# Optimization experiments

Measured on AMD Instinct MI355X. Metric: run time of the kernel, lower is better.

## Reference

```python
import jax, jax.numpy as jnp
import numpy as np

NUM_EMBEDDINGS = 256
EMBEDDING_DIM = 8


def setup_inputs() -> dict:
    key = jax.random.key(0)
    ks = jax.random.split(key, 8)
    B, D_in, H, D_out = 1024, 512, 2048, 512
    s = lambda fan: 1.0 / np.sqrt(fan)
    return {
        "x": jax.random.normal(ks[0], (B, D_in), dtype=jnp.float32),
        "emb_W": jax.random.normal(ks[1], (NUM_EMBEDDINGS, EMBEDDING_DIM), dtype=jnp.float32),
        "W_in": jax.random.normal(ks[2], (H, D_in), dtype=jnp.float32) * s(D_in),
        "b_in": jax.random.normal(ks[3], (H,), dtype=jnp.float32) * s(D_in),
        "W_h": jax.random.normal(ks[4], (H, H), dtype=jnp.float32) * s(H),
        "b_h": jax.random.normal(ks[5], (H,), dtype=jnp.float32) * s(H),
        "W_out": jax.random.normal(ks[6], (D_out, H), dtype=jnp.float32) * s(H),
        "b_out": jax.random.normal(ks[7], (D_out,), dtype=jnp.float32) * s(H),
    }


def reference(x, emb_W, W_in, b_in, W_h, b_h, W_out, b_out):
    B, D_in = x.shape
    flat = x.reshape(-1)  # [B*D_in], row-major flatten == torch .flatten()
    # power-feature expansion: powers 1..embedding_dim stacked on axis 1
    exps = jnp.arange(1, EMBEDDING_DIM + 1, dtype=x.dtype)
    x_res = flat[:, None] ** exps[None, :]  # [B*D_in, E]
    # get_ind: NOTE source uses sum(flat_x) (not sum of squares) -- faithful
    sm = jnp.sum(x_res, axis=1, keepdims=True)              # [N,1]
    emb = jnp.sum(emb_W * emb_W, axis=1)[None, :]           # [1,K]
    dist = sm + emb - 2.0 * (x_res @ emb_W.T)               # [N,K]
    ind = jnp.argmin(dist, axis=1)                          # [N] int
    # q = ind.view_as(x.T).T : reshape to [D_in, B] then transpose
    q = ind.reshape(D_in, B).T.astype(x.dtype)              # [B, D_in]
    # straight-through: forward value q, gradient flows to x
    q = x + jax.lax.stop_gradient(q - x)
    relu = jax.nn.relu
    h = relu(q @ W_in.T + b_in)      # d_in
    for _ in range(4):               # shared d_h applied 4 times
        h = relu(h @ W_h.T + b_h)
    f = relu(h @ W_out.T + b_out)    # d_out
    q_latent_loss = jnp.float32(0.0)  # eval mode
    return (f, q_latent_loss)
```

## Files before the change

### kernel.cpp

```cpp
#include <hip/hip_runtime.h>
#include <hip/hip_bf16.h>
#include <math.h>


#define B_ROWS 1024
#define D_IN   512
#define HDIM   2048
#define NTOT   (B_ROWS * D_IN)
#define NCODE  256
#define EDIM   8

typedef __attribute__((ext_vector_type(8))) short bf16x8;
typedef __attribute__((ext_vector_type(4))) float f32x4;

__device__ inline void gload_lds16(const void* g, void* l) {
    __builtin_amdgcn_global_load_lds(
        (const __attribute__((address_space(1))) void*)g,
        (__attribute__((address_space(3))) void*)l, 16, 0, 0);
}

__device__ inline ushort bf16_hi_bits(float v, float* hi_f) {
    __hip_bfloat16 h = __float2bfloat16(v);
    *hi_f = __bfloat162float(h);
    ushort u; __builtin_memcpy(&u, &h, 2); return u;
}
__device__ inline ushort bf16_bits(float v) {
    __hip_bfloat16 h = __float2bfloat16(v);
    ushort u; __builtin_memcpy(&u, &h, 2); return u;
}

__global__ __launch_bounds__(256) void quantize_kernel(
    const float* __restrict__ x, const float* __restrict__ embW,
    ushort* __restrict__ qhi, float* __restrict__ loss_out)
{
    __shared__ float sW[NCODE][EDIM];
    __shared__ float sE[NCODE];

    const int tid = threadIdx.x;
    for (int i = tid; i < NCODE * EDIM; i += 256)
        ((float*)sW)[i] = embW[i];
    __syncthreads();
    {
        const float* w = sW[tid];
        float s0 = __fmul_rn(w[0], w[0]), s1 = __fmul_rn(w[1], w[1]);
        float s2 = __fmul_rn(w[2], w[2]), s3 = __fmul_rn(w[3], w[3]);
        float s4 = __fmul_rn(w[4], w[4]), s5 = __fmul_rn(w[5], w[5]);
        float s6 = __fmul_rn(w[6], w[6]), s7 = __fmul_rn(w[7], w[7]);
        float a = __fadd_rn(__fadd_rn(s0, s1), __fadd_rn(s2, s3));
        float b = __fadd_rn(__fadd_rn(s4, s5), __fadd_rn(s6, s7));
        sE[tid] = __fadd_rn(a, b);
    }
    __syncthreads();

    const int n = blockIdx.x * 256 + tid;
    const float v = x[n];

    float p[EDIM];
    #pragma unroll
    for (int e = 0; e < EDIM; ++e)
        p[e] = powf(v, (float)(e + 1));

    float sm;
    {
        float a = __fadd_rn(__fadd_rn(p[0], p[1]), __fadd_rn(p[2], p[3]));
        float b = __fadd_rn(__fadd_rn(p[4], p[5]), __fadd_rn(p[6], p[7]));
        sm = __fadd_rn(a, b);
    }

    float best = INFINITY;
    int bi = 0;
    for (int k = 0; k < NCODE; ++k) {
        const float4 w0 = *reinterpret_cast<const float4*>(&sW[k][0]);
        const float4 w1 = *reinterpret_cast<const float4*>(&sW[k][4]);
        float dot = 0.f;
        dot = fmaf(p[0], w0.x, dot); dot = fmaf(p[1], w0.y, dot);
        dot = fmaf(p[2], w0.z, dot); dot = fmaf(p[3], w0.w, dot);
        dot = fmaf(p[4], w1.x, dot); dot = fmaf(p[5], w1.y, dot);
        dot = fmaf(p[6], w1.z, dot); dot = fmaf(p[7], w1.w, dot);
        float d = __fsub_rn(__fadd_rn(sm, sE[k]), __fmul_rn(2.0f, dot));
        if (d < best) { best = d; bi = k; }
    }

    const int bo = n & (B_ROWS - 1);
    const int dd = n >> 10;
    qhi[bo * D_IN + dd] = bf16_bits((float)bi);

    if (blockIdx.x == 0 && tid == 0) loss_out[0] = 0.0f;
}

__global__ __launch_bounds__(256) void split_all(
    const float* __restrict__ Wi, const float* __restrict__ Wh,
    const float* __restrict__ Wo,
    ushort* __restrict__ wihi, ushort* __restrict__ wilo,
    ushort* __restrict__ whhi, ushort* __restrict__ whlo,
    ushort* __restrict__ wohi, ushort* __restrict__ wolo)
{
    const int i = blockIdx.x * 256 + threadIdx.x;
    const int R0 = HDIM * D_IN / 4;
    const int R1 = R0 + HDIM * HDIM / 4;
    const float* src; ushort* hi; ushort* lo; int j;
    if (i < R0)      { src = Wi; hi = wihi; lo = wilo; j = i; }
    else if (i < R1) { src = Wh; hi = whhi; lo = whlo; j = i - R0; }
    else             { src = Wo; hi = wohi; lo = wolo; j = i - R1; }
    float4 v = reinterpret_cast<const float4*>(src)[j];
    float f[4] = {v.x, v.y, v.z, v.w};
    ushort hh[4], ll[4];
    #pragma unroll
    for (int c = 0; c < 4; ++c) {
        float hf;
        hh[c] = bf16_hi_bits(f[c], &hf);
        ll[c] = bf16_bits(f[c] - hf);
    }
    ushort4 h = {hh[0], hh[1], hh[2], hh[3]};
    ushort4 l = {ll[0], ll[1], ll[2], ll[3]};
    reinterpret_cast<ushort4*>(hi)[j] = h;
    reinterpret_cast<ushort4*>(lo)[j] = l;
}

template<bool ALO, bool PARTIAL>
__global__ __launch_bounds__(256) void gemm_split(
    const ushort* __restrict__ Ahi, const ushort* __restrict__ Alo,
    const ushort* __restrict__ Whi, const ushort* __restrict__ Wlo,
    const float* __restrict__ bias,
    ushort* __restrict__ Ohi, ushort* __restrict__ Olo,
    float* __restrict__ OF, int N, int K, int klen)
{
    constexpr int BUF = 49152;
    constexpr int OFF_AH = 0, OFF_AL = 8192, OFF_BH = 16384;
    __shared__ char lds[2 * BUF];

    const int tid = threadIdx.x, lane = tid & 63, wid = tid >> 6;

    const int gy = gridDim.y;
    const int nwg = gridDim.x * gy;
    int lin = blockIdx.x * gy + blockIdx.y;
    int q   = nwg >> 3;
    int sw  = (lin & 7) * q + (lin >> 3);
    int bx  = sw / gy, by2 = sw % gy;
    const int bm   = (by2 & 15) << 6;
    const int kz   = by2 >> 4;
    const int kbeg = kz * klen;
    const int bn   = bx << 7;

    const int wm = (wid >> 1) << 5;
    const int wn = (wid & 1) << 6;

    constexpr int NSEGW = ALO ? 12 : 10;
    const ushort* gp[NSEGW];
    uint ldsoff[NSEGW];
    #pragma unroll
    for (int i = 0; i < NSEGW; ++i) {
        int s = wid + i * 4;
        const ushort* pl; int row0, base, sip;
        if (ALO) {
            if (s < 8)       { pl = Ahi; row0 = bm; base = OFF_AH;         sip = s; }
            else if (s < 16) { pl = Alo; row0 = bm; base = OFF_AL;         sip = s - 8; }
            else if (s < 32) { pl = Whi; row0 = bn; base = OFF_BH;         sip = s - 16; }
            else             { pl = Wlo; row0 = bn; base = OFF_BH + 16384; sip = s - 32; }
        } else {
            if (s < 8)       { pl = Ahi; row0 = bm; base = OFF_AH;         sip = s; }
            else if (s < 24) { pl = Whi; row0 = bn; base = OFF_BH;         sip = s - 8; }
            else             { pl = Wlo; row0 = bn; base = OFF_BH + 16384; sip = s - 24; }
        }
        int r  = sip * 8 + (lane >> 3);
        int ch = (lane & 7) ^ (r & 7);
        gp[i]     = pl + (size_t)(row0 + r) * K + kbeg + ch * 8;
        ldsoff[i] = base + sip * 1024;
    }

    uint aoff[2][2], boff[4][2];
    #pragma unroll
    for (int f = 0; f < 2; ++f) {
        int ar = wm + f * 16 + (lane & 15);
        #pragma unroll
        for (int s = 0; s < 2; ++s) {
            int ch = (s * 4 + (lane >> 4)) ^ (ar & 7);
            aoff[f][s] = OFF_AH + ar * 128 + ch * 16;
        }
    }
    #pragma unroll
    for (int f = 0; f < 4; ++f) {
        int br = wn + f * 16 + (lane & 15);
        #pragma unroll
        for (int s = 0; s < 2; ++s) {
            int ch = (s * 4 + (lane >> 4)) ^ (br & 7);
            boff[f][s] = OFF_BH + br * 128 + ch * 16;
        }
    }

    auto stage = [&](int kt, int b) {
        #pragma unroll
        for (int i = 0; i < NSEGW; ++i)
            gload_lds16(gp[i] + kt * 64, lds + b * BUF + ldsoff[i]);
    };

    f32x4 acc[2][4] = {};
    const int NT = klen >> 6;

    stage(0, 0);
    __syncthreads();

    for (int t = 0; t < NT; ++t) {
        const int cur = t & 1;
        if (t + 1 < NT) stage(t + 1, cur ^ 1);

        const char* lb = lds + cur * BUF;
        bf16x8 aH[2][2], aL[2][2], bH[2][4], bL[2][4];
        #pragma unroll
        for (int s = 0; s < 2; ++s) {
            #pragma unroll
            for (int f = 0; f < 2; ++f) {
                aH[s][f] = *(const bf16x8*)(lb + aoff[f][s]);
                if constexpr (ALO) aL[s][f] = *(const bf16x8*)(lb + aoff[f][s] + 8192);
            }
            #pragma unroll
            for (int f = 0; f < 4; ++f) {
                bH[s][f] = *(const bf16x8*)(lb + boff[f][s]);
                bL[s][f] = *(const bf16x8*)(lb + boff[f][s] + 16384);
            }
        }
        #pragma unroll
        for (int s = 0; s < 2; ++s) {
            #pragma unroll
            for (int fm = 0; fm < 2; ++fm)
                #pragma unroll
                for (int fn = 0; fn < 4; ++fn)
                    acc[fm][fn] = __builtin_amdgcn_mfma_f32_16x16x32_bf16(
                        aH[s][fm], bH[s][fn], acc[fm][fn], 0, 0, 0);
            #pragma unroll
            for (int fm = 0; fm < 2; ++fm)
                #pragma unroll
                for (int fn = 0; fn < 4; ++fn)
                    acc[fm][fn] = __builtin_amdgcn_mfma_f32_16x16x32_bf16(
                        aH[s][fm], bL[s][fn], acc[fm][fn], 0, 0, 0);
            if constexpr (ALO) {
                #pragma unroll
                for (int fm = 0; fm < 2; ++fm)
                    #pragma unroll
                    for (int fn = 0; fn < 4; ++fn)
                        acc[fm][fn] = __builtin_amdgcn_mfma_f32_16x16x32_bf16(
                            aL[s][fm], bH[s][fn], acc[fm][fn], 0, 0, 0);
            }
        }
        __syncthreads();
    }

    #pragma unroll
    for (int fm = 0; fm < 2; ++fm) {
        #pragma unroll
        for (int fn = 0; fn < 4; ++fn) {
            const int col = bn + wn + fn * 16 + (lane & 15);
            const int rb  = bm + wm + fm * 16 + ((lane >> 4) << 2);
            if constexpr (PARTIAL) {
                #pragma unroll
                for (int r = 0; r < 4; ++r)
                    OF[(size_t)(kz * B_ROWS + rb + r) * N + col] = acc[fm][fn][r];
            } else {
                const float bc = bias[col];
                #pragma unroll
                for (int r = 0; r < 4; ++r) {
                    float v = acc[fm][fn][r] + bc;
                    v = v > 0.f ? v : 0.f;
                    float hf;
                    ushort hb = bf16_hi_bits(v, &hf);
                    Ohi[(size_t)(rb + r) * N + col] = hb;
                    Olo[(size_t)(rb + r) * N + col] = bf16_bits(v - hf);
                }
            }
        }
    }
}

__global__ __launch_bounds__(256) void combine_relu(
    const float* __restrict__ part, const float* __restrict__ bias,
    float* __restrict__ out)
{
    const int i = blockIdx.x * 256 + threadIdx.x;
    const float4* p = (const float4*)part;
    float4 a = p[i], b = p[i + 131072], c = p[i + 262144], d = p[i + 393216];
    float4 bb = ((const float4*)bias)[i & 127];
    float4 o;
    o.x = a.x + b.x + c.x + d.x + bb.x;
    o.y = a.y + b.y + c.y + d.y + bb.y;
    o.z = a.z + b.z + c.z + d.z + bb.z;
    o.w = a.w + b.w + c.w + d.w + bb.w;
    o.x = o.x > 0.f ? o.x : 0.f;
    o.y = o.y > 0.f ? o.y : 0.f;
    o.z = o.z > 0.f ? o.z : 0.f;
    o.w = o.w > 0.f ? o.w : 0.f;
    reinterpret_cast<float4*>(out)[i] = o;
}

extern "C" void kernel_launch(void* const* d_in, const int* in_sizes, int n_in,
                              void* d_out, int out_size, void* d_ws, size_t ws_size,
                              hipStream_t stream)
{
    const float* x     = (const float*)d_in[0];
    const float* emb_W = (const float*)d_in[1];
    const float* W_in  = (const float*)d_in[2];
    const float* b_in  = (const float*)d_in[3];
    const float* W_h   = (const float*)d_in[4];
    const float* b_h   = (const float*)d_in[5];
    const float* W_out = (const float*)d_in[6];
    const float* b_out = (const float*)d_in[7];
    float* out = (float*)d_out;

    char* w = (char*)d_ws;
    const size_t MB = 1 << 20;
    ushort* qhi  = (ushort*)(w);
    ushort* h1hi = (ushort*)(w + 1*MB);
    ushort* h1lo = (ushort*)(w + 5*MB);
    ushort* h2hi = (ushort*)(w + 9*MB);
    ushort* h2lo = (ushort*)(w + 13*MB);
    float*  partial = (float*)(w + 9*MB);
    ushort* wihi = (ushort*)(w + 17*MB);
    ushort* wilo = (ushort*)(w + 19*MB);
    ushort* whhi = (ushort*)(w + 21*MB);
    ushort* whlo = (ushort*)(w + 29*MB);
    ushort* wohi = (ushort*)(w + 37*MB);
    ushort* wolo = (ushort*)(w + 39*MB);

    split_all<<<6144, 256, 0, stream>>>(W_in, W_h, W_out,
                                        wihi, wilo, whhi, whlo, wohi, wolo);

    quantize_kernel<<<NTOT / 256, 256, 0, stream>>>(x, emb_W, qhi, out + NTOT);

    gemm_split<false, false><<<dim3(16, 16), 256, 0, stream>>>(
        qhi, nullptr, wihi, wilo, b_in, h1hi, h1lo, nullptr, HDIM, D_IN, D_IN);

    ushort *shi = h1hi, *slo = h1lo, *dhi = h2hi, *dlo = h2lo;
    for (int l = 0; l < 4; ++l) {
        gemm_split<true, false><<<dim3(16, 16), 256, 0, stream>>>(
            shi, slo, whhi, whlo, b_h, dhi, dlo, nullptr, HDIM, HDIM, HDIM);
        ushort* t;
        t = shi; shi = dhi; dhi = t;
        t = slo; slo = dlo; dlo = t;
    }

    gemm_split<true, true><<<dim3(4, 64), 256, 0, stream>>>(
        shi, slo, wohi, wolo, nullptr, nullptr, nullptr, partial, D_IN, HDIM, D_IN);

    combine_relu<<<512, 256, 0, stream>>>(partial, b_out, out);
}
```

Before: 224.3 us.

## Fuse quantize with weight split, split-K hidden GEMMs with new 128x128 tile kernel

The quantize kernel and the W_in/W_h hi/lo bf16 split now share one launch, and each quantize thread handles two elements with the factor 2 folded into the powers. The hidden layers use a new gemm_mid kernel with a 64-wide K tile and 2-way split-K, followed by a combine kernel that adds bias, applies ReLU and re-splits to hi/lo. W_out splitting moves to a separate small kernel and the final layer also goes through gemm_mid. This is meant to raise hidden-layer parallelism and cut launch count, at the cost of extra fp32 partial traffic and four more combine launches.

```diff
diff --git a/kernel.cpp b/kernel.cpp
--- a/kernel.cpp
+++ b/kernel.cpp
@@ -29,92 +29,124 @@
     ushort u; __builtin_memcpy(&u, &h, 2); return u;
 }
 
-__global__ __launch_bounds__(256) void quantize_kernel(
+__global__ __launch_bounds__(256) void fused_pre(
     const float* __restrict__ x, const float* __restrict__ embW,
-    ushort* __restrict__ qhi, float* __restrict__ loss_out)
-{
-    __shared__ float sW[NCODE][EDIM];
-    __shared__ float sE[NCODE];
-
+    const float* __restrict__ Wi, const float* __restrict__ Wh,
+    ushort* __restrict__ qhi,
+    ushort* __restrict__ wihi, ushort* __restrict__ wilo,
+    ushort* __restrict__ whhi, ushort* __restrict__ whlo,
+    float* __restrict__ loss_out)
+{
+    __shared__ float sWE[NCODE][12];
     const int tid = threadIdx.x;
-    for (int i = tid; i < NCODE * EDIM; i += 256)
-        ((float*)sW)[i] = embW[i];
-    __syncthreads();
+
+    if (blockIdx.x >= 1024) {
+        const int sidx = blockIdx.x - 1024;
+        #pragma unroll
+        for (int s = 0; s < 4; ++s) {
+            const int g = sidx * 1024 + s * 256 + tid;
+            const float* src; ushort* hi; ushort* lo; int j;
+            if (g < 262144) { src = Wi; hi = wihi; lo = wilo; j = g; }
+            else            { src = Wh; hi = whhi; lo = whlo; j = g - 262144; }
+            float4 v = reinterpret_cast<const float4*>(src)[j];
+            float f[4] = {v.x, v.y, v.z, v.w};
+            ushort hh[4], ll[4];
+            #pragma unroll
+            for (int c = 0; c < 4; ++c) {
+                float hf;
+                hh[c] = bf16_hi_bits(f[c], &hf);
+                ll[c] = bf16_bits(f[c] - hf);
+            }
+            ushort4 h4 = {hh[0], hh[1], hh[2], hh[3]};
+            ushort4 l4 = {ll[0], ll[1], ll[2], ll[3]};
+            reinterpret_cast<ushort4*>(hi)[j] = h4;
+            reinterpret_cast<ushort4*>(lo)[j] = l4;
+        }
+        return;
+    }
+
     {
-        const float* w = sW[tid];
-        float s0 = __fmul_rn(w[0], w[0]), s1 = __fmul_rn(w[1], w[1]);
-        float s2 = __fmul_rn(w[2], w[2]), s3 = __fmul_rn(w[3], w[3]);
-        float s4 = __fmul_rn(w[4], w[4]), s5 = __fmul_rn(w[5], w[5]);
-        float s6 = __fmul_rn(w[6], w[6]), s7 = __fmul_rn(w[7], w[7]);
+        const float4 a4 = *reinterpret_cast<const float4*>(&embW[tid * EDIM]);
+        const float4 b4 = *reinterpret_cast<const float4*>(&embW[tid * EDIM + 4]);
+        float s0 = __fmul_rn(a4.x, a4.x), s1 = __fmul_rn(a4.y, a4.y);
+        float s2 = __fmul_rn(a4.z, a4.z), s3 = __fmul_rn(a4.w, a4.w);
+        float s4 = __fmul_rn(b4.x, b4.x), s5 = __fmul_rn(b4.y, b4.y);
+        float s6 = __fmul_rn(b4.z, b4.z), s7 = __fmul_rn(b4.w, b4.w);
         float a = __fadd_rn(__fadd_rn(s0, s1), __fadd_rn(s2, s3));
         float b = __fadd_rn(__fadd_rn(s4, s5), __fadd_rn(s6, s7));
-        sE[tid] = __fadd_rn(a, b);
+        sWE[tid][0] = a4.x; sWE[tid][1] = a4.y; sWE[tid][2] = a4.z; sWE[tid][3] = a4.w;
+        sWE[tid][4] = b4.x; sWE[tid][5] = b4.y; sWE[tid][6] = b4.z; sWE[tid][7] = b4.w;
+        sWE[tid][8] = __fadd_rn(a, b);
     }
     __syncthreads();
 
-    const int n = blockIdx.x * 256 + tid;
-    const float v = x[n];
-
-    float p[EDIM];
-    #pragma unroll
-    for (int e = 0; e < EDIM; ++e)
-        p[e] = powf(v, (float)(e + 1));
-
-    float sm;
-    {
+    const int nbase = blockIdx.x * 512 + tid;
+
+    float p2[2][EDIM], sm[2];
+    #pragma unroll
+    for (int j = 0; j < 2; ++j) {
+        const float v = x[nbase + j * 256];
+        float p[EDIM];
+        #pragma unroll
+        for (int e = 0; e < EDIM; ++e)
+            p[e] = powf(v, (float)(e + 1));
         float a = __fadd_rn(__fadd_rn(p[0], p[1]), __fadd_rn(p[2], p[3]));
         float b = __fadd_rn(__fadd_rn(p[4], p[5]), __fadd_rn(p[6], p[7]));
-        sm = __fadd_rn(a, b);
-    }
-
-    float best = INFINITY;
-    int bi = 0;
+        sm[j] = __fadd_rn(a, b);
+        #pragma unroll
+        for (int e = 0; e < EDIM; ++e)
+            p2[j][e] = 2.0f * p[e];
+    }
+
+    float best[2] = {INFINITY, INFINITY};
+    int   bi[2]   = {0, 0};
     for (int k = 0; k < NCODE; ++k) {
-        const float4 w0 = *reinterpret_cast<const float4*>(&sW[k][0]);
-        const float4 w1 = *reinterpret_cast<const float4*>(&sW[k][4]);
-        float dot = 0.f;
-        dot = fmaf(p[0], w0.x, dot); dot = fmaf(p[1], w0.y, dot);
-        dot = fmaf(p[2], w0.z, dot); dot = fmaf(p[3], w0.w, dot);
-        dot = fmaf(p[4], w1.x, dot); dot = fmaf(p[5], w1.y, dot);
-        dot = fmaf(p[6], w1.z, dot); dot = fmaf(p[7], w1.w, dot);
-        float d = __fsub_rn(__fadd_rn(sm, sE[k]), __fmul_rn(2.0f, dot));
-        if (d < best) { best = d; bi = k; }
-    }
-
-    const int bo = n & (B_ROWS - 1);
-    const int dd = n >> 10;
-    qhi[bo * D_IN + dd] = bf16_bits((float)bi);
-
+        const float4 w0 = *reinterpret_cast<const float4*>(&sWE[k][0]);
+        const float4 w1 = *reinterpret_cast<const float4*>(&sWE[k][4]);
+        const float  Ek = sWE[k][8];
+        #pragma unroll
+        for (int j = 0; j < 2; ++j) {
+            float dot = 0.f;
+            dot = fmaf(p2[j][0], w0.x, dot); dot = fmaf(p2[j][1], w0.y, dot);
+            dot = fmaf(p2[j][2], w0.z, dot); dot = fmaf(p2[j][3], w0.w, dot);
+            dot = fmaf(p2[j][4], w1.x, dot); dot = fmaf(p2[j][5], w1.y, dot);
+            dot = fmaf(p2[j][6], w1.z, dot); dot = fmaf(p2[j][7], w1.w, dot);
+            float d = __fsub_rn(__fadd_rn(sm[j], Ek), dot);
+            if (d < best[j]) { best[j] = d; bi[j] = k; }
+        }
+    }
+
+    #pragma unroll
+    for (int j = 0; j < 2; ++j) {
+        const int n  = nbase + j * 256;
+        const int bo = n & (B_ROWS - 1);
+        const int dd = n >> 10;
+        qhi[bo * D_IN + dd] = bf16_bits((float)bi[j]);
+    }
     if (blockIdx.x == 0 && tid == 0) loss_out[0] = 0.0f;
 }
 
-__global__ __launch_bounds__(256) void split_all(
-    const float* __restrict__ Wi, const float* __restrict__ Wh,
-    const float* __restrict__ Wo,
-    ushort* __restrict__ wihi, ushort* __restrict__ wilo,
-    ushort* __restrict__ whhi, ushort* __restrict__ whlo,
-    ushort* __restrict__ wohi, ushort* __restrict__ wolo)
-{
-    const int i = blockIdx.x * 256 + threadIdx.x;
-    const int R0 = HDIM * D_IN / 4;
-    const int R1 = R0 + HDIM * HDIM / 4;
-    const float* src; ushort* hi; ushort* lo; int j;
-    if (i < R0)      { src = Wi; hi = wihi; lo = wilo; j = i; }
-    else if (i < R1) { src = Wh; hi = whhi; lo = whlo; j = i - R0; }
-    else             { src = Wo; hi = wohi; lo = wolo; j = i - R1; }
-    float4 v = reinterpret_cast<const float4*>(src)[j];
-    float f[4] = {v.x, v.y, v.z, v.w};
-    ushort hh[4], ll[4];
-    #pragma unroll
-    for (int c = 0; c < 4; ++c) {
-        float hf;
-        hh[c] = bf16_hi_bits(f[c], &hf);
-        ll[c] = bf16_bits(f[c] - hf);
-    }
-    ushort4 h = {hh[0], hh[1], hh[2], hh[3]};
-    ushort4 l = {ll[0], ll[1], ll[2], ll[3]};
-    reinterpret_cast<ushort4*>(hi)[j] = h;
-    reinterpret_cast<ushort4*>(lo)[j] = l;
+__global__ __launch_bounds__(256) void wo_split(
+    const float* __restrict__ Wo, ushort* __restrict__ hi, ushort* __restrict__ lo)
+{
+    const int tid = threadIdx.x;
+    #pragma unroll
+    for (int s = 0; s < 4; ++s) {
+        const int j = blockIdx.x * 1024 + s * 256 + tid;
+        float4 v = reinterpret_cast<const float4*>(Wo)[j];
+        float f[4] = {v.x, v.y, v.z, v.w};
+        ushort hh[4], ll[4];
+        #pragma unroll
+        for (int c = 0; c < 4; ++c) {
+            float hf;
+            hh[c] = bf16_hi_bits(f[c], &hf);
+            ll[c] = bf16_bits(f[c] - hf);
+        }
+        ushort4 h4 = {hh[0], hh[1], hh[2], hh[3]};
+        ushort4 l4 = {ll[0], ll[1], ll[2], ll[3]};
+        reinterpret_cast<ushort4*>(hi)[j] = h4;
+        reinterpret_cast<ushort4*>(lo)[j] = l4;
+    }
 }
 
 template<bool ALO, bool PARTIAL>
@@ -269,6 +301,148 @@
             }
         }
     }
+}
+
+__global__ __launch_bounds__(256) void gemm_mid(
+    const ushort* __restrict__ Ahi, const ushort* __restrict__ Alo,
+    const ushort* __restrict__ Bhi, const ushort* __restrict__ Blo,
+    float* __restrict__ OF, int N, int Kfull, int klen)
+{
+    constexpr int BUF = 65536;
+    constexpr int OFF_A[2] = {0, 16384};
+    constexpr int OFF_B[2] = {32768, 49152};
+    __shared__ char lds[2 * BUF];
+
+    const int tid = threadIdx.x, lane = tid & 63, wid = tid >> 6;
+
+    const int gy = gridDim.y;
+    const int nwg = gridDim.x * gy;
+    int lin = blockIdx.x * gy + blockIdx.y;
+    int q   = nwg >> 3;
+    int sw  = (lin & 7) * q + (lin >> 3);
+    int bx  = sw / gy, by2 = sw % gy;
+    const int bm   = (by2 & 7) << 7;
+    const int kz   = by2 >> 3;
+    const int kbeg = kz * klen;
+    const int bn   = bx << 7;
+
+    const int wm = (wid >> 1) << 6;
+    const int wn = (wid & 1) << 6;
+
+    const int ch0 = (lane & 7) ^ (lane >> 3);
+    const size_t kstep8 = (size_t)Kfull * 8;
+    const ushort* gpb[4];
+    uint lob[4];
+    {
+        const ushort* pls[4] = {Ahi, Alo, Bhi, Blo};
+        const int row0s[4]   = {bm, bm, bn, bn};
+        const uint bases[4]  = {OFF_A[0], OFF_A[1], OFF_B[0], OFF_B[1]};
+        #pragma unroll
+        for (int p = 0; p < 4; ++p) {
+            gpb[p] = pls[p] + (size_t)(row0s[p] + wid * 32 + (lane >> 3)) * Kfull
+                     + kbeg + ch0 * 8;
+            lob[p] = bases[p] + wid * 4096;
+        }
+    }
+
+    uint aoff[4][2], boff[4][2];
+    #pragma unroll
+    for (int f = 0; f < 4; ++f) {
+        #pragma unroll
+        for (int ks = 0; ks < 2; ++ks) {
+            int ch = (ks * 4 + (lane >> 4)) ^ (lane & 7);
+            aoff[f][ks] = OFF_A[0] + (wm + f * 16 + (lane & 15)) * 128 + ch * 16;
+            boff[f][ks] = OFF_B[0] + (wn + f * 16 + (lane & 15)) * 128 + ch * 16;
+        }
+    }
+
+    auto stage = [&](int kt, int b) {
+        #pragma unroll
+        for (int p = 0; p < 4; ++p)
+            #pragma unroll
+            for (int i = 0; i < 4; ++i)
+                gload_lds16(gpb[p] + i * kstep8 + kt * 64,
+                            lds + b * BUF + lob[p] + i * 1024);
+    };
+
+    f32x4 acc[4][4] = {};
+    const int NT = klen >> 6;
+
+    stage(0, 0);
+    __syncthreads();
+
+    for (int t = 0; t < NT; ++t) {
+        const int cur = t & 1;
+        if (t + 1 < NT) stage(t + 1, cur ^ 1);
+
+        const char* lb = lds + cur * BUF;
+        #pragma unroll
+        for (int ks = 0; ks < 2; ++ks) {
+            bf16x8 aH[4], aL[4], bH[4], bL[4];
+            #pragma unroll
+            for (int f = 0; f < 4; ++f) {
+                aH[f] = *(const bf16x8*)(lb + aoff[f][ks]);
+                aL[f] = *(const bf16x8*)(lb + aoff[f][ks] + 16384);
+                bH[f] = *(const bf16x8*)(lb + boff[f][ks]);
+                bL[f] = *(const bf16x8*)(lb + boff[f][ks] + 16384);
+            }
+            #pragma unroll
+            for (int fm = 0; fm < 4; ++fm)
+                #pragma unroll
+                for (int fn = 0; fn < 4; ++fn)
+                    acc[fm][fn] = __builtin_amdgcn_mfma_f32_16x16x32_bf16(
+                        aH[fm], bH[fn], acc[fm][fn], 0, 0, 0);
+            #pragma unroll
+            for (int fm = 0; fm < 4; ++fm)
+                #pragma unroll
+                for (int fn = 0; fn < 4; ++fn)
+                    acc[fm][fn] = __builtin_amdgcn_mfma_f32_16x16x32_bf16(
+                        aH[fm], bL[fn], acc[fm][fn], 0, 0, 0);
+            #pragma unroll
+            for (int fm = 0; fm < 4; ++fm)
+                #pragma unroll
+                for (int fn = 0; fn < 4; ++fn)
+                    acc[fm][fn] = __builtin_amdgcn_mfma_f32_16x16x32_bf16(
+                        aL[fm], bH[fn], acc[fm][fn], 0, 0, 0);
+        }
+        __syncthreads();
+    }
+
+    #pragma unroll
+    for (int fm = 0; fm < 4; ++fm) {
+        #pragma unroll
+        for (int fn = 0; fn < 4; ++fn) {
+            const int col = bn + wn + fn * 16 + (lane & 15);
+            const int rb  = bm + wm + fm * 16 + ((lane >> 4) << 2);
+            #pragma unroll
+            for (int r = 0; r < 4; ++r)
+                OF[(size_t)(kz * B_ROWS + rb + r) * N + col] = acc[fm][fn][r];
+        }
+    }
+}
+
+__global__ __launch_bounds__(256) void combine_mid(
+    const float* __restrict__ part, const float* __restrict__ bias,
+    ushort* __restrict__ hi, ushort* __restrict__ lo)
+{
+    const int i = blockIdx.x * 256 + threadIdx.x;
+    const float4* p = (const float4*)part;
+    float4 a = p[i], b = p[i + 524288];
+    float4 bb = ((const float4*)bias)[i & 511];
+    float f[4] = {a.x + b.x + bb.x, a.y + b.y + bb.y,
+                  a.z + b.z + bb.z, a.w + b.w + bb.w};
+    ushort hh[4], ll[4];
+    #pragma unroll
+    for (int c = 0; c < 4; ++c) {
+        float v = f[c] > 0.f ? f[c] : 0.f;
+        float hf;
+        hh[c] = bf16_hi_bits(v, &hf);
+        ll[c] = bf16_bits(v - hf);
+    }
+    ushort4 h4 = {hh[0], hh[1], hh[2], hh[3]};
+    ushort4 l4 = {ll[0], ll[1], ll[2], ll[3]};
+    reinterpret_cast<ushort4*>(hi)[i] = h4;
+    reinterpret_cast<ushort4*>(lo)[i] = l4;
 }
 
 __global__ __launch_bounds__(256) void combine_relu(
@@ -307,38 +481,34 @@
 
     char* w = (char*)d_ws;
     const size_t MB = 1 << 20;
-    ushort* qhi  = (ushort*)(w);
-    ushort* h1hi = (ushort*)(w + 1*MB);
-    ushort* h1lo = (ushort*)(w + 5*MB);
-    ushort* h2hi = (ushort*)(w + 9*MB);
-    ushort* h2lo = (ushort*)(w + 13*MB);
-    float*  partial = (float*)(w + 9*MB);
-    ushort* wihi = (ushort*)(w + 17*MB);
-    ushort* wilo = (ushort*)(w + 19*MB);
-    ushort* whhi = (ushort*)(w + 21*MB);
-    ushort* whlo = (ushort*)(w + 29*MB);
-    ushort* wohi = (ushort*)(w + 37*MB);
-    ushort* wolo = (ushort*)(w + 39*MB);
-
-    split_all<<<6144, 256, 0, stream>>>(W_in, W_h, W_out,
-                                        wihi, wilo, whhi, whlo, wohi, wolo);
-
-    quantize_kernel<<<NTOT / 256, 256, 0, stream>>>(x, emb_W, qhi, out + NTOT);
+    ushort* qhi    = (ushort*)(w);
+    ushort* wihi   = (ushort*)(w + 1*MB);
+    ushort* wilo   = (ushort*)(w + 3*MB);
+    float*  midpar = (float*)(w);
+    ushort* wohi   = (ushort*)(w);
+    ushort* wolo   = (ushort*)(w + 2*MB);
+    float*  l6par  = (float*)(w + 4*MB);
+    ushort* hhi    = (ushort*)(w + 16*MB);
+    ushort* hlo    = (ushort*)(w + 20*MB);
+    ushort* whhi   = (ushort*)(w + 24*MB);
+    ushort* whlo   = (ushort*)(w + 32*MB);
+
+    fused_pre<<<2304, 256, 0, stream>>>(x, emb_W, W_in, W_h,
+                                        qhi, wihi, wilo, whhi, whlo, out + NTOT);
 
     gemm_split<false, false><<<dim3(16, 16), 256, 0, stream>>>(
-        qhi, nullptr, wihi, wilo, b_in, h1hi, h1lo, nullptr, HDIM, D_IN, D_IN);
-
-    ushort *shi = h1hi, *slo = h1lo, *dhi = h2hi, *dlo = h2lo;
+        qhi, nullptr, wihi, wilo, b_in, hhi, hlo, nullptr, HDIM, D_IN, D_IN);
+
     for (int l = 0; l < 4; ++l) {
-        gemm_split<true, false><<<dim3(16, 16), 256, 0, stream>>>(
-            shi, slo, whhi, whlo, b_h, dhi, dlo, nullptr, HDIM, HDIM, HDIM);
-        ushort* t;
-        t = shi; shi = dhi; dhi = t;
-        t = slo; slo = dlo; dlo = t;
-    }
-
-    gemm_split<true, true><<<dim3(4, 64), 256, 0, stream>>>(
-        shi, slo, wohi, wolo, nullptr, nullptr, nullptr, partial, D_IN, HDIM, D_IN);
-
-    combine_relu<<<512, 256, 0, stream>>>(partial, b_out, out);
-}
+        gemm_mid<<<dim3(16, 16), 256, 0, stream>>>(
+            hhi, hlo, whhi, whlo, midpar, HDIM, HDIM, 1024);
+        combine_mid<<<2048, 256, 0, stream>>>(midpar, b_h, hhi, hlo);
+    }
+
+    wo_split<<<256, 256, 0, stream>>>(W_out, wohi, wolo);
+
+    gemm_mid<<<dim3(4, 32), 256, 0, stream>>>(
+        hhi, hlo, wohi, wolo, l6par, D_IN, HDIM, D_IN);
+
+    combine_relu<<<512, 256, 0, stream>>>(l6par, b_out, out);
+}
```

Measured after the change: 217.7 us. -2.9%, faster.
